# Kernel tuning notes

Hardware: AMD Instinct MI355X
Metric: run time of the kernel (lower is better)

Reference implementation:

```python
import jax, jax.numpy as jnp
import numpy as np

B, C, H, W = 16, 512, 32, 32
NH = 8
HD = C // NH  # 64


def setup_inputs() -> dict:
    key = jax.random.key(0)
    ks = jax.random.split(key, 9)
    s = 1.0 / np.sqrt(C)
    return {
        "x": jax.random.normal(ks[0], (B, C, H, W), dtype=jnp.float32),
        "Wq": jax.random.normal(ks[1], (C, C), dtype=jnp.float32) * s,
        "bq": jnp.zeros((C,), dtype=jnp.float32),
        "Wk": jax.random.normal(ks[2], (C, C), dtype=jnp.float32) * s,
        "bk": jnp.zeros((C,), dtype=jnp.float32),
        "Wv": jax.random.normal(ks[3], (C, C), dtype=jnp.float32) * s,
        "bv": jnp.zeros((C,), dtype=jnp.float32),
        "Wo": jax.random.normal(ks[4], (C, C), dtype=jnp.float32) * s,
        "bo": jnp.zeros((C,), dtype=jnp.float32),
    }


def reference(x, Wq, bq, Wk, bk, Wv, bv, Wo, bo):
    b, c, h, w = x.shape
    n = h * w  # sequence of spatial tokens
    # [B, C, H, W] -> [B, N, C]
    xf = x.reshape(b, c, n).transpose(0, 2, 1)
    # separate QKV projections, split heads: [B, NH, N, HD]
    def split_heads(t):
        return t.reshape(b, n, NH, HD).transpose(0, 2, 1, 3)
    q = split_heads(xf @ Wq + bq)
    k = split_heads(xf @ Wk + bk)
    v = split_heads(xf @ Wv + bv)
    # energy: [B, NH, N, N]
    energy = jnp.einsum('bhqd,bhkd->bhqk', q, k) / jnp.sqrt(jnp.float32(HD))
    attn = jax.nn.softmax(energy, axis=-1)
    out = jnp.einsum('bhqk,bhkd->bhqd', attn, v)  # [B, NH, N, HD]
    out = out.transpose(0, 2, 1, 3).reshape(b, n, c)
    out = out @ Wo + bo
    return out.transpose(0, 2, 1).reshape(b, c, h, w)
```

## Files before the change

### kernel.cpp

```cpp
#include <hip/hip_runtime.h>
#include <hip/hip_bf16.h>
#include <math.h>

constexpr int B_  = 16;
constexpr int C_  = 512;
constexpr int N_  = 1024;
constexpr int NH_ = 8;
constexpr int HD_ = 64;

#define QSCALE 0.18033688f

typedef __attribute__((ext_vector_type(8))) short short8;
typedef __attribute__((ext_vector_type(4))) short short4v;
typedef __attribute__((ext_vector_type(4))) float f32x4;
#define MFMA16(a, b, c) __builtin_amdgcn_mfma_f32_16x16x32_bf16((a), (b), (c), 0, 0, 0)

#if __has_builtin(__builtin_amdgcn_exp2f)
#define EXP2(x) __builtin_amdgcn_exp2f(x)
#else
#define EXP2(x) exp2f(x)
#endif

__device__ __forceinline__ short f2bf(float f) {
    union { float f; unsigned u; } a; a.f = f;
    unsigned r = a.u + 0x7fffu + ((a.u >> 16) & 1u);
    return (short)(r >> 16);
}
__device__ __forceinline__ short f2bf_hw(float f) {
    __hip_bfloat16 h = __float2bfloat16(f);
    return *reinterpret_cast<short*>(&h);
}

__device__ __forceinline__ void gload_lds16(const void* g, void* l) {
    __builtin_amdgcn_global_load_lds(
        (const __attribute__((address_space(1))) unsigned*)g,
        (__attribute__((address_space(3))) unsigned*)l, 16, 0, 0);
}

__global__ __launch_bounds__(256) void prep_all(
    const float* __restrict__ x, short* __restrict__ xt,
    const float* __restrict__ Wq, const float* __restrict__ Wk,
    const float* __restrict__ Wv, const float* __restrict__ Wo,
    short* __restrict__ WqT, short* __restrict__ WkT,
    short* __restrict__ WvT, short* __restrict__ WoT) {
    __shared__ float t[64][65];
    const int tid = threadIdx.x;
    const int wgid = blockIdx.x;
    if (wgid < 2048) {
        const int xcd = wgid & 7;
        const int i = wgid >> 3;
        const int b  = 2 * xcd + (i >= 128);
        const int tile = i & 127;
        const int tn = tile >> 3;
        const int tc = tile & 7;
        #pragma unroll
        for (int k = 0; k < 16; ++k) {
            int idx = k * 256 + tid;
            int r = idx >> 6, col = idx & 63;
            t[r][col] = x[((size_t)b * C_ + tc * 64 + r) * N_ + tn * 64 + col];
        }
        __syncthreads();
        #pragma unroll
        for (int k = 0; k < 16; ++k) {
            int idx = k * 256 + tid;
            int r2 = idx >> 6, col2 = idx & 63;
            xt[((size_t)b * N_ + tn * 64 + r2) * C_ + tc * 64 + col2] = f2bf(t[col2][r2]);
        }
    } else {
        const int idx0 = wgid - 2048;
        const int z = idx0 >> 6;
        const float* W = (z == 0) ? Wq : (z == 1) ? Wk : (z == 2) ? Wv : Wo;
        short* WT      = (z == 0) ? WqT : (z == 1) ? WkT : (z == 2) ? WvT : WoT;
        const int tile = idx0 & 63;
        const int tco = tile >> 3;
        const int tc  = tile & 7;
        #pragma unroll
        for (int i = 0; i < 16; ++i) {
            int idx = i * 256 + tid;
            int r = idx >> 6, col = idx & 63;
            t[r][col] = W[((size_t)tc * 64 + r) * C_ + tco * 64 + col];
        }
        __syncthreads();
        #pragma unroll
        for (int i = 0; i < 16; ++i) {
            int idx = i * 256 + tid;
            int r2 = idx >> 6, col2 = idx & 63;
            WT[((size_t)tco * 64 + r2) * C_ + tc * 64 + col2] = f2bf(t[col2][r2]);
        }
    }
}

#define GEMM_STAGE(buf, t)                                                    \
    {                                                                         \
        _Pragma("unroll")                                                     \
        for (int ii = 0; ii < 4; ++ii) {                                      \
            gload_lds16(Ag + arowoff + (size_t)ii * 8 * C_ + (t) * 64,        \
                        &smem[buf][0][wave * 32 + ii * 8][0]);                \
            gload_lds16(Bg + arowoff + (size_t)ii * 8 * C_ + (t) * 64,        \
                        &smem[buf][1][wave * 32 + ii * 8][0]);                \
        }                                                                     \
    }

#define GEMM_CORE()                                                           \
    GEMM_STAGE(0, 0);                                                         \
    __syncthreads();                                                          \
    for (int t = 0; t < 8; ++t) {                                             \
        const int buf = t & 1;                                                \
        if (t < 7) GEMM_STAGE(buf ^ 1, t + 1);                                \
        __builtin_amdgcn_s_setprio(1);                                        \
        _Pragma("unroll")                                                     \
        for (int ks = 0; ks < 2; ++ks) {                                      \
            short8 af[4], bf[4];                                              \
            const int sw = ((ks * 4 + g) ^ (c & 7)) << 3;                     \
            _Pragma("unroll")                                                 \
            for (int fm = 0; fm < 4; ++fm)                                    \
                af[fm] = *(const short8*)&smem[buf][0][wm * 64 + fm * 16 + c][sw]; \
            _Pragma("unroll")                                                 \
            for (int fn = 0; fn < 4; ++fn)                                    \
                bf[fn] = *(const short8*)&smem[buf][1][wn * 64 + fn * 16 + c][sw]; \
            _Pragma("unroll")                                                 \
            for (int fm = 0; fm < 4; ++fm)                                    \
                _Pragma("unroll")                                             \
                for (int fn = 0; fn < 4; ++fn)                                \
                    acc[fm][fn] = MFMA16(af[fm], bf[fn], acc[fm][fn]);        \
        }                                                                     \
        __builtin_amdgcn_s_setprio(0);                                        \
        __syncthreads();                                                      \
    }

__global__ __launch_bounds__(256) void qkv_mfma(
    const short* __restrict__ xt,
    const short* __restrict__ WqT, const float* __restrict__ bq,
    const short* __restrict__ WkT, const float* __restrict__ bk,
    const short* __restrict__ WvT, const float* __restrict__ bv,
    short* __restrict__ Qs, short* __restrict__ Kb, short* __restrict__ Vt) {
    const int wgid = blockIdx.x;
    const int xcd = wgid & 7;
    const int i = wgid >> 3;
    const int b = 2 * xcd + (i >= 96);
    const int rem = (i >= 96) ? i - 96 : i;
    const int z = rem >> 5;
    const int tile = rem & 31;
    const int mt = tile >> 2;
    const int nt = tile & 3;
    const int tid = threadIdx.x;
    const int wave = tid >> 6, lane = tid & 63;
    const int g = lane >> 4, c = lane & 15;
    const int wm = wave >> 1, wn = wave & 1;

    const short* W    = (z == 0) ? WqT : (z == 1) ? WkT : WvT;
    const float* bias = (z == 0) ? bq  : (z == 1) ? bk  : bv;

    __shared__ __align__(16) short smem[2][2][128][64];

    const short* Ag = xt + (size_t)b * N_ * C_ + (size_t)mt * 128 * C_;
    const short* Bg = W + (size_t)nt * 128 * C_;

    const int lrow = lane >> 3, lslot = lane & 7;
    const size_t arowoff = (size_t)(wave * 32 + lrow) * C_ + ((lslot ^ lrow) << 3);

    f32x4 acc[4][4] = {};
    GEMM_CORE();

    const int tok0 = mt * 128 + wm * 64;
    const int co0  = nt * 128 + wn * 64;
    const int h = co0 >> 6;
    const size_t bh = (size_t)(b * NH_ + h);

    if (z < 2) {
        short* Y = (z == 0) ? Qs : Kb;
        const float sc = (z == 0) ? QSCALE : 1.f;
        #pragma unroll
        for (int fm = 0; fm < 4; ++fm)
            #pragma unroll
            for (int fn = 0; fn < 4; ++fn)
                #pragma unroll
                for (int r = 0; r < 4; ++r) {
                    int tok = tok0 + fm * 16 + 4 * g + r;
                    int hd  = fn * 16 + c;
                    float v = (acc[fm][fn][r] + bias[co0 + hd]) * sc;
                    Y[(bh * N_ + tok) * HD_ + hd] = f2bf_hw(v);
                }
    } else {
        short (*t72)[72] = (short(*)[72])((short*)smem + wave * 32 * 72);
        #pragma unroll
        for (int p = 0; p < 2; ++p) {
            #pragma unroll
            for (int fn2 = 0; fn2 < 2; ++fn2) {
                int fnn = 2 * p + fn2;
                #pragma unroll
                for (int fm = 0; fm < 4; ++fm) {
                    short4v pk;
                    #pragma unroll
                    for (int r = 0; r < 4; ++r)
                        pk[r] = f2bf_hw(acc[fm][fnn][r] + bias[co0 + fnn * 16 + c]);
                    *(short4v*)&t72[fn2 * 16 + c][fm * 16 + 4 * g] = pk;
                }
            }
            int row = lane >> 1, half2 = lane & 1;
            int hd = p * 32 + row;
            size_t base = (bh * HD_ + hd) * N_ + tok0 + half2 * 32;
            #pragma unroll
            for (int j = 0; j < 4; ++j)
                *(short8*)&Vt[base + j * 8] = *(const short8*)&t72[row][half2 * 32 + j * 8];
        }
    }
}

__global__ __launch_bounds__(512) void attn_mfma(
    const short* __restrict__ Qs, const short* __restrict__ Kb,
    const short* __restrict__ Vt, short* __restrict__ Ah) {
    const int wgid = blockIdx.x;
    const int swz  = (wgid & 7) * 64 + (wgid >> 3);
    const int b  = swz >> 5;
    const int h  = (swz >> 2) & 7;
    const int qt = swz & 3;
    const int tid = threadIdx.x;
    const int wave = tid >> 6, lane = tid & 63;
    const int g = lane >> 4, c = lane & 15;
    const int q0 = qt * 256 + wave * 32;
    const size_t bh = (size_t)(b * NH_ + h);

    const short* Qw  = Qs + (bh * N_ + q0) * HD_;
    const short* Kbb = Kb + bh * N_ * HD_;
    const short* Vtb = Vt + bh * HD_ * N_;

    __shared__ short KV[2][2][4096];
    __shared__ short Pl[8][32][64];
    short (*P)[64] = Pl[wave];
    const int px = (c & 7) << 1;

    const int srow = tid >> 3;
    const int sc16 = tid & 7;
    const int kdst = srow * 64 + 8 * (sc16 ^ (srow & 7));
    short8 gk, gv;

    #define STAGE_LOAD(key0)                                                   \
        do {                                                                   \
            gk = *(const short8*)&Kbb[(size_t)((key0) + srow) * HD_ + sc16 * 8]; \
            gv = *(const short8*)&Vtb[(size_t)srow * N_ + (key0) + sc16 * 8];    \
        } while (0)
    #define STAGE_WRITE(buf)                                                   \
        do {                                                                   \
            *(short8*)&KV[buf][0][kdst] = gk;                                  \
            *(short8*)&KV[buf][1][kdst] = gv;                                  \
        } while (0)

    short8 qf[2][2];
    #pragma unroll
    for (int f = 0; f < 2; ++f)
        #pragma unroll
        for (int k0 = 0; k0 < 2; ++k0)
            qf[f][k0] = *(const short8*)&Qw[(f * 16 + c) * HD_ + k0 * 32 + g * 8];

    short8 ones8;
    #pragma unroll
    for (int j = 0; j < 8; ++j) ones8[j] = (short)0x3F80;

    f32x4 o[2][4] = {};
    f32x4 lacc[2] = {};

    STAGE_LOAD(0);
    STAGE_WRITE(0);
    STAGE_LOAD(64);
    __syncthreads();

    int cur = 0;
    for (int it = 0; it < 16; ++it) {
        if (it < 15) STAGE_WRITE(cur ^ 1);
        if (it < 14) STAGE_LOAD((it + 2) * 64);

        const short* Kl = &KV[cur][0][0];
        const short* Vl = &KV[cur][1][0];

        f32x4 s[2][4] = {};
        __builtin_amdgcn_s_setprio(1);
        #pragma unroll
        for (int m = 0; m < 4; ++m) {
            const int row = m * 16 + c;
            short8 ka = *(const short8*)&Kl[row * 64 + 8 * ((g)     ^ (row & 7))];
            short8 kb = *(const short8*)&Kl[row * 64 + 8 * ((4 + g) ^ (row & 7))];
            s[0][m] = MFMA16(ka, qf[0][0], s[0][m]);
            s[0][m] = MFMA16(kb, qf[0][1], s[0][m]);
            s[1][m] = MFMA16(ka, qf[1][0], s[1][m]);
            s[1][m] = MFMA16(kb, qf[1][1], s[1][m]);
        }
        __builtin_amdgcn_s_setprio(0);

        #pragma unroll
        for (int f = 0; f < 2; ++f) {
            #pragma unroll
            for (int m = 0; m < 4; ++m) {
                short4v pk;
                #pragma unroll
                for (int r = 0; r < 4; ++r) pk[r] = f2bf_hw(EXP2(s[f][m][r]));
                *(short4v*)&P[f * 16 + c][((4 * m + g) ^ px) * 4] = pk;
            }
        }

        short8 pa[2][2];
        #pragma unroll
        for (int f = 0; f < 2; ++f)
            #pragma unroll
            for (int k0 = 0; k0 < 2; ++k0)
                pa[f][k0] = *(const short8*)&P[f * 16 + c][((k0 * 8 + 2 * g) ^ px) * 4];
        __builtin_amdgcn_s_setprio(1);
        lacc[0] = MFMA16(pa[0][0], ones8, lacc[0]);
        lacc[0] = MFMA16(pa[0][1], ones8, lacc[0]);
        lacc[1] = MFMA16(pa[1][0], ones8, lacc[1]);
        lacc[1] = MFMA16(pa[1][1], ones8, lacc[1]);
        #pragma unroll
        for (int n = 0; n < 4; ++n) {
            const int row = n * 16 + c;
            short8 va = *(const short8*)&Vl[row * 64 + 8 * ((g)     ^ (row & 7))];
            short8 vb = *(const short8*)&Vl[row * 64 + 8 * ((4 + g) ^ (row & 7))];
            o[0][n] = MFMA16(pa[0][0], va, o[0][n]);
            o[0][n] = MFMA16(pa[0][1], vb, o[0][n]);
            o[1][n] = MFMA16(pa[1][0], va, o[1][n]);
            o[1][n] = MFMA16(pa[1][1], vb, o[1][n]);
        }
        __builtin_amdgcn_s_setprio(0);

        __syncthreads();
        cur ^= 1;
    }
    #undef STAGE_LOAD
    #undef STAGE_WRITE

    #pragma unroll
    for (int f = 0; f < 2; ++f) {
        float li[4];
        #pragma unroll
        for (int r = 0; r < 4; ++r) li[r] = 1.f / lacc[f][r];
        #pragma unroll
        for (int n = 0; n < 4; ++n)
            #pragma unroll
            for (int r = 0; r < 4; ++r) {
                int tok = q0 + f * 16 + 4 * g + r;
                int cc  = h * 64 + n * 16 + c;
                Ah[((size_t)b * N_ + tok) * C_ + cc] = f2bf_hw(o[f][n][r] * li[r]);
            }
    }
}

__global__ __launch_bounds__(256) void proj_mfma(
    const short* __restrict__ Ah, const short* __restrict__ WoT,
    const float* __restrict__ bo, float* __restrict__ out) {
    const int wgid = blockIdx.x;
    const int xcd = wgid & 7;
    const int i = wgid >> 3;
    const int b = 2 * xcd + (i >= 32);
    const int tile = i & 31;
    const int mt = tile >> 2;
    const int nt = tile & 3;
    const int tid = threadIdx.x;
    const int wave = tid >> 6, lane = tid & 63;
    const int g = lane >> 4, c = lane & 15;
    const int wm = wave >> 1, wn = wave & 1;

    __shared__ __align__(16) short smem[2][2][128][64];

    const short* Ag = Ah + (size_t)b * N_ * C_ + (size_t)mt * 128 * C_;
    const short* Bg = WoT + (size_t)nt * 128 * C_;

    const int lrow = lane >> 3, lslot = lane & 7;
    const size_t arowoff = (size_t)(wave * 32 + lrow) * C_ + ((lslot ^ lrow) << 3);

    f32x4 acc[4][4] = {};
    GEMM_CORE();

    const int tok0 = mt * 128 + wm * 64;
    const int co0  = nt * 128 + wn * 64;

    float (*tf)[68] = (float(*)[68])((float*)smem + wave * 32 * 68);
    #pragma unroll
    for (int p = 0; p < 2; ++p) {
        #pragma unroll
        for (int fm = 0; fm < 4; ++fm)
            #pragma unroll
            for (int fn2 = 0; fn2 < 2; ++fn2) {
                float4 v = *(float4*)&acc[fm][2 * p + fn2];
                *(float4*)&tf[fn2 * 16 + c][fm * 16 + 4 * g] = v;
            }
        int row = lane >> 1, half = lane & 1;
        int co = co0 + p * 32 + row;
        float bias = bo[co];
        float* ob = out + ((size_t)b * C_ + co) * N_ + tok0 + half * 32;
        #pragma unroll
        for (int j = 0; j < 8; ++j) {
            float4 v = *(const float4*)&tf[row][half * 32 + j * 4];
            v.x += bias; v.y += bias; v.z += bias; v.w += bias;
            *(float4*)&ob[j * 4] = v;
        }
    }
}

extern "C" void kernel_launch(void* const* d_in, const int* in_sizes, int n_in,
                              void* d_out, int out_size, void* d_ws, size_t ws_size,
                              hipStream_t stream) {
    (void)in_sizes; (void)n_in; (void)out_size; (void)ws_size;
    const float* x  = (const float*)d_in[0];
    const float* Wq = (const float*)d_in[1];
    const float* bq = (const float*)d_in[2];
    const float* Wk = (const float*)d_in[3];
    const float* bk = (const float*)d_in[4];
    const float* Wv = (const float*)d_in[5];
    const float* bv = (const float*)d_in[6];
    const float* Wo = (const float*)d_in[7];
    const float* bo = (const float*)d_in[8];
    float* out = (float*)d_out;

    char* ws = (char*)d_ws;
    const size_t MB = 1024 * 1024;
    short* xt  = (short*)(ws + 0 * MB);
    short* WqT = (short*)(ws + 16 * MB);
    short* WkT = (short*)(ws + 16 * MB + 512 * 1024);
    short* WvT = (short*)(ws + 17 * MB);
    short* WoT = (short*)(ws + 17 * MB + 512 * 1024);
    short* Qsb = (short*)(ws + 18 * MB);
    short* Kb  = (short*)(ws + 34 * MB);
    short* Vt  = (short*)(ws + 50 * MB);
    short* Ah  = (short*)(ws + 66 * MB);

    prep_all<<<dim3(2304), 256, 0, stream>>>(x, xt, Wq, Wk, Wv, Wo,
                                             WqT, WkT, WvT, WoT);
    qkv_mfma<<<dim3(1536), 256, 0, stream>>>(xt, WqT, bq, WkT, bk, WvT, bv,
                                             Qsb, Kb, Vt);
    attn_mfma<<<dim3(512), 512, 0, stream>>>(Qsb, Kb, Vt, Ah);
    proj_mfma<<<dim3(512), 256, 0, stream>>>(Ah, WoT, bo, out);
}
```

Baseline: 108.6 us.

## Enlarge QKV GEMM tiles to 128x256 with 8 waves and triple-buffered LDS

The QKV projection kernel moves from 128x128 tiles with 4 waves to 128x256 tiles with 8 waves, halving the grid. Its K loop becomes a 3-stage LDS ring with 32-wide K slices, direct global-to-LDS loads and explicit vmcnt waits plus one barrier per step. The aim is more reuse of the activation tile across output columns and better overlap of loads with MFMA. In exchange there are fewer workgroups for the CUs, and the V transpose path now needs an extra sync before it reuses LDS.

```diff
diff --git a/kernel.cpp b/kernel.cpp
--- a/kernel.cpp
+++ b/kernel.cpp
@@ -128,7 +128,7 @@
         __syncthreads();                                                      \
     }
 
-__global__ __launch_bounds__(256) void qkv_mfma(
+__global__ __launch_bounds__(512) void qkv_mfma(
     const short* __restrict__ xt,
     const short* __restrict__ WqT, const float* __restrict__ bq,
     const short* __restrict__ WkT, const float* __restrict__ bk,
@@ -137,33 +137,75 @@
     const int wgid = blockIdx.x;
     const int xcd = wgid & 7;
     const int i = wgid >> 3;
-    const int b = 2 * xcd + (i >= 96);
-    const int rem = (i >= 96) ? i - 96 : i;
-    const int z = rem >> 5;
-    const int tile = rem & 31;
-    const int mt = tile >> 2;
-    const int nt = tile & 3;
+    const int b = 2 * xcd + (i >= 48);
+    const int rem = (i >= 48) ? i - 48 : i;
+    const int z = rem >> 4;
+    const int tile = rem & 15;
+    const int mt = tile >> 1;
+    const int nt = tile & 1;
     const int tid = threadIdx.x;
     const int wave = tid >> 6, lane = tid & 63;
     const int g = lane >> 4, c = lane & 15;
-    const int wm = wave >> 1, wn = wave & 1;
+    const int wm = wave >> 2;
+    const int wn = wave & 3;
 
     const short* W    = (z == 0) ? WqT : (z == 1) ? WkT : WvT;
     const float* bias = (z == 0) ? bq  : (z == 1) ? bk  : bv;
 
-    __shared__ __align__(16) short smem[2][2][128][64];
+    __shared__ __align__(16) short smem3[3][384][32];
 
     const short* Ag = xt + (size_t)b * N_ * C_ + (size_t)mt * 128 * C_;
-    const short* Bg = W + (size_t)nt * 128 * C_;
-
-    const int lrow = lane >> 3, lslot = lane & 7;
-    const size_t arowoff = (size_t)(wave * 32 + lrow) * C_ + ((lslot ^ lrow) << 3);
+    const short* Bg = W + (size_t)nt * 256 * C_;
+
+    const int srow  = tid >> 2;
+    const int sslot = (tid & 3) ^ ((srow >> 2) & 3);
+
+    #define QKV_STAGE(s, kt)                                                  \
+        do {                                                                  \
+            const int kk_ = (kt) * 32;                                        \
+            gload_lds16(Ag + (size_t)srow * C_ + kk_ + sslot * 8,             \
+                        &smem3[s][wave * 16][0]);                             \
+            gload_lds16(Bg + (size_t)srow * C_ + kk_ + sslot * 8,             \
+                        &smem3[s][128 + wave * 16][0]);                       \
+            gload_lds16(Bg + (size_t)(128 + srow) * C_ + kk_ + sslot * 8,     \
+                        &smem3[s][256 + wave * 16][0]);                       \
+        } while (0)
 
     f32x4 acc[4][4] = {};
-    GEMM_CORE();
+    const int rsw = (g ^ (c >> 2)) * 8;
+
+    QKV_STAGE(0, 0);
+    QKV_STAGE(1, 1);
+    asm volatile("s_waitcnt vmcnt(3)" ::: "memory");
+    __builtin_amdgcn_s_barrier();
+
+    int sR = 0, sN = 1, sS = 2;
+    for (int t = 0; t < 16; ++t) {
+        if (t < 14) QKV_STAGE(sS, t + 2);
+        const short (*S)[32] = smem3[sR];
+        short8 af[4], bf[4];
+        #pragma unroll
+        for (int fm = 0; fm < 4; ++fm)
+            af[fm] = *(const short8*)&S[wm * 64 + fm * 16 + c][rsw];
+        #pragma unroll
+        for (int fn = 0; fn < 4; ++fn)
+            bf[fn] = *(const short8*)&S[128 + wn * 64 + fn * 16 + c][rsw];
+        __builtin_amdgcn_s_setprio(1);
+        #pragma unroll
+        for (int fm = 0; fm < 4; ++fm)
+            #pragma unroll
+            for (int fn = 0; fn < 4; ++fn)
+                acc[fm][fn] = MFMA16(af[fm], bf[fn], acc[fm][fn]);
+        __builtin_amdgcn_s_setprio(0);
+        if (t < 14)       { asm volatile("s_waitcnt vmcnt(3)" ::: "memory"); }
+        else if (t == 14) { asm volatile("s_waitcnt vmcnt(0)" ::: "memory"); }
+        if (t < 15) __builtin_amdgcn_s_barrier();
+        int tmp = sR; sR = sN; sN = sS; sS = tmp;
+    }
+    #undef QKV_STAGE
 
     const int tok0 = mt * 128 + wm * 64;
-    const int co0  = nt * 128 + wn * 64;
+    const int co0  = nt * 256 + wn * 64;
     const int h = co0 >> 6;
     const size_t bh = (size_t)(b * NH_ + h);
 
@@ -182,7 +224,8 @@
                     Y[(bh * N_ + tok) * HD_ + hd] = f2bf_hw(v);
                 }
     } else {
-        short (*t72)[72] = (short(*)[72])((short*)smem + wave * 32 * 72);
+        __syncthreads();
+        short (*t72)[72] = (short(*)[72])((short*)smem3 + wave * 32 * 72);
         #pragma unroll
         for (int p = 0; p < 2; ++p) {
             #pragma unroll
@@ -424,8 +467,8 @@
 
     prep_all<<<dim3(2304), 256, 0, stream>>>(x, xt, Wq, Wk, Wv, Wo,
                                              WqT, WkT, WvT, WoT);
-    qkv_mfma<<<dim3(1536), 256, 0, stream>>>(xt, WqT, bq, WkT, bk, WvT, bv,
-                                             Qsb, Kb, Vt);
+    qkv_mfma<<<dim3(768), 512, 0, stream>>>(xt, WqT, bq, WkT, bk, WvT, bv,
+                                            Qsb, Kb, Vt);
     attn_mfma<<<dim3(512), 512, 0, stream>>>(Qsb, Kb, Vt, Ah);
     proj_mfma<<<dim3(512), 256, 0, stream>>>(Ah, WoT, bo, out);
 }
```

Measured after the change: 109.6 us. Within noise of the previous version (+0.9%).
